# Optimization experiments

Hardware: AMD Instinct MI355X
Metric: run time of the kernel (lower is better)

## Reference

```python
import jax, jax.numpy as jnp
import numpy as np
import math

N_EMBD = 384
N_HEAD = 6
HEAD_DIM = N_EMBD // N_HEAD  # 64
EPS = 1e-5


def apply_rotary_emb(x, cos, sin):
    # x: [B, T, H, D]; cos/sin: [1, T, 1, D//2]
    d = x.shape[3] // 2
    x1, x2 = x[..., :d], x[..., d:]
    y1 = x1 * cos + x2 * sin
    y2 = -x1 * sin + x2 * cos
    return jnp.concatenate([y1, y2], axis=3).astype(x.dtype)


def rms_norm(x):
    # no learned gain, eps inside the sqrt's argument as in the torch code
    return x * jax.lax.rsqrt(jnp.mean(x * x, axis=-1, keepdims=True) + EPS)


def setup_inputs() -> dict:
    key = jax.random.key(0)
    ks = jax.random.split(key, 7)
    B, T = 8, 2048
    x = jax.random.normal(ks[0], (B, T, N_EMBD), dtype=jnp.float32)
    scale = 1.0 / math.sqrt(N_EMBD)
    Wq = jax.random.normal(ks[1], (N_EMBD, N_EMBD), dtype=jnp.float32) * scale
    Wk = jax.random.normal(ks[2], (N_EMBD, N_EMBD), dtype=jnp.float32) * scale
    Wv = jax.random.normal(ks[3], (N_EMBD, N_EMBD), dtype=jnp.float32) * scale
    Wo = jax.random.normal(ks[4], (N_EMBD, N_EMBD), dtype=jnp.float32) * scale
    # RoPE tables: true cos/sin of position*inv_freq
    half = HEAD_DIM // 2
    inv_freq = 1.0 / (10000.0 ** (jnp.arange(half, dtype=jnp.float32) / half))
    t = jnp.arange(T, dtype=jnp.float32)
    freqs = t[:, None] * inv_freq[None, :]  # [T, half]
    cos = jnp.cos(freqs)[None, :, None, :]  # [1, T, 1, half]
    sin = jnp.sin(freqs)[None, :, None, :]
    return {"x": x, "Wq": Wq, "Wk": Wk, "Wv": Wv, "Wo": Wo, "cos": cos, "sin": sin}


def reference(x, Wq, Wk, Wv, Wo, cos, sin):
    B, T, C = x.shape
    H, D = N_HEAD, HEAD_DIM
    # torch Linear: y = x @ W.T (weights stored [out, in])
    q = (x @ Wq.T).reshape(B, T, H, D)
    k = (x @ Wk.T).reshape(B, T, H, D)
    v = (x @ Wv.T).reshape(B, T, H, D)
    q = apply_rotary_emb(q, cos, sin)
    k = apply_rotary_emb(k, cos, sin)
    q = rms_norm(q)
    k = rms_norm(k)
    # attention: [B, H, T, T] scores, full softmax (no causal mask in source)
    att = jnp.einsum("bthd,bshd->bhts", q, k) * (1.0 / math.sqrt(D))
    att = jax.nn.softmax(att, axis=-1)
    y = jnp.einsum("bhts,bshd->bthd", att, v).reshape(B, T, C)
    return y @ Wo.T
```

## Files before the change

### kernel.cpp

```cpp
#include <hip/hip_runtime.h>
#include <hip/hip_bf16.h>
#include <stdint.h>

#define B_ 8
#define T_ 2048
#define C_ 384
#define H_ 6
#define D_ 64
#define M_ (B_*T_)

typedef unsigned short u16;
typedef unsigned int u32;
typedef __attribute__((ext_vector_type(8))) short short8;
typedef __attribute__((ext_vector_type(4))) float floatx4;
typedef __attribute__((ext_vector_type(16))) float floatx16;

#define QSCALE 0.18033688011112042f

__device__ __forceinline__ u16 f2b(float f) {
  union { float f; unsigned u; } x; x.f = f;
  unsigned r = x.u + 0x7fffu + ((x.u >> 16) & 1u);
  return (u16)(r >> 16);
}
__device__ __forceinline__ u32 pack_bf16(float a, float b) {
  union { __hip_bfloat162 h; u32 u; } x;
  x.h = __float22bfloat162_rn(float2{a, b});
  return x.u;
}
__device__ __forceinline__ uint4 pack8(const float4& lo, const float4& hi) {
  uint4 r;
  r.x = pack_bf16(lo.x, lo.y); r.y = pack_bf16(lo.z, lo.w);
  r.z = pack_bf16(hi.x, hi.y); r.w = pack_bf16(hi.z, hi.w);
  return r;
}

__device__ __forceinline__ void plswap(u32& a, u32& b) {
  asm("v_permlane32_swap_b32 %0, %1" : "+v"(a), "+v"(b));
}

__device__ __forceinline__ float fexp2(float x) {
#if __has_builtin(__builtin_amdgcn_exp2f)
  return __builtin_amdgcn_exp2f(x);
#else
  float r; asm("v_exp_f32 %0, %1" : "=v"(r) : "v"(x)); return r;
#endif
}

__device__ __forceinline__ u32 cvtpk(float a, float b) {
  u32 r; asm("v_cvt_pk_bf16_f32 %0, %1, %2" : "=v"(r) : "v"(a), "v"(b)); return r;
}

__device__ __forceinline__ void gl_lds16(const u16* g, u16* l) {
#if __has_builtin(__builtin_amdgcn_global_load_lds)
  __builtin_amdgcn_global_load_lds(
      (const __attribute__((address_space(1))) unsigned int*)g,
      (__attribute__((address_space(3))) unsigned int*)l,
      16, 0, 0);
#else
  *reinterpret_cast<uint4*>(l + (threadIdx.x & 63) * 8) =
      *reinterpret_cast<const uint4*>(g);
#endif
}

__global__ __launch_bounds__(256) void prep_bf16(
    const float* __restrict__ x,
    const float* __restrict__ wq, const float* __restrict__ wk,
    const float* __restrict__ wv, const float* __restrict__ wo,
    u16* __restrict__ xb,
    u16* __restrict__ wqb, u16* __restrict__ wkb,
    u16* __restrict__ wvb, u16* __restrict__ wob)
{
  const int c = blockIdx.x * 256 + threadIdx.x;
  const float* src;
  u16* dst;
  int off;
  if (c < 786432) {
    src = x; dst = xb; off = c;
  } else {
    int t = c - 786432;
    int wsel = t / 18432;
    off = t - wsel * 18432;
    src = (wsel == 0) ? wq : (wsel == 1) ? wk : (wsel == 2) ? wv : wo;
    dst = (wsel == 0) ? wqb : (wsel == 1) ? wkb : (wsel == 2) ? wvb : wob;
  }
  const float4* p = reinterpret_cast<const float4*>(src + (size_t)off * 8);
  float4 lo = p[0], hi = p[1];
  *reinterpret_cast<uint4*>(dst + (size_t)off * 8) = pack8(lo, hi);
}

__global__ __launch_bounds__(256) void qkv_fused(
    const u16* __restrict__ Xb,
    const u16* __restrict__ Wqb, const u16* __restrict__ Wkb, const u16* __restrict__ Wvb,
    const float* __restrict__ cosb, const float* __restrict__ sinb,
    u16* __restrict__ Qo, u16* __restrict__ Ko, u16* __restrict__ Vto)
{
  __shared__ __align__(16) u16 smem[128 * 64 + 3 * 64 * 64];
  u16* As = smem;
  u16* Bs0 = smem + 128 * 64;

  const int id = blockIdx.x;
  const int xcd = id & 7;
  const int s = id >> 3;
  const int mb = xcd * 16 + s / 6;
  const int hh = s % 6;
  const int m0 = mb * 128;
  const int n0 = hh * 64;

  const int tid = threadIdx.x;
  const int w = tid >> 6;
  const int lane = tid & 63;
  const int quad = lane >> 4;
  const int c = lane & 15;

  const u16* Wz[3] = {Wqb, Wkb, Wvb};

  floatx4 acc[3][2][4];
#pragma unroll
  for (int z = 0; z < 3; z++)
#pragma unroll
    for (int i = 0; i < 2; i++)
#pragma unroll
      for (int j = 0; j < 4; j++) acc[z][i][j] = (floatx4){0.f, 0.f, 0.f, 0.f};

  const int lrow = lane >> 3;
  const int lcol = (lane & 7) * 8;

  for (int k0 = 0; k0 < 384; k0 += 64) {
    __syncthreads();
#pragma unroll
    for (int n = 0; n < 4; n++) {
      const int ch = w * 4 + n;
      gl_lds16(Xb + (size_t)(m0 + ch * 8 + lrow) * C_ + k0 + lcol, As + ch * 512);
    }
#pragma unroll
    for (int z = 0; z < 3; z++)
#pragma unroll
      for (int n = 0; n < 2; n++) {
        const int ch = w * 2 + n;
        gl_lds16(Wz[z] + (size_t)(n0 + ch * 8 + lrow) * C_ + k0 + lcol,
                 Bs0 + z * 4096 + ch * 512);
      }
    __syncthreads();

#pragma unroll
    for (int ks = 0; ks < 2; ks++) {
      short8 af2[2];
#pragma unroll
      for (int mi = 0; mi < 2; mi++)
        af2[mi] = *reinterpret_cast<const short8*>(
            As + (w * 32 + mi * 16 + c) * 64 + (ks * 4 + quad) * 8);
#pragma unroll
      for (int z = 0; z < 3; z++) {
#pragma unroll
        for (int ni = 0; ni < 4; ni++) {
          short8 bf = *reinterpret_cast<const short8*>(
              Bs0 + z * 4096 + (ni * 16 + c) * 64 + (ks * 4 + quad) * 8);
#pragma unroll
          for (int mi = 0; mi < 2; mi++)
            acc[z][mi][ni] = __builtin_amdgcn_mfma_f32_16x16x32_bf16(af2[mi], bf, acc[z][mi][ni], 0, 0, 0);
        }
      }
    }
  }

  const int bb2 = m0 >> 11;
  const int tbase = m0 & (T_ - 1);

  {
    const size_t vbase = ((size_t)(bb2 * H_ + hh)) * D_ * T_;
#pragma unroll
    for (int mi = 0; mi < 2; mi++) {
      int t = tbase + w * 32 + mi * 16 + quad * 4;
#pragma unroll
      for (int ni = 0; ni < 4; ni++) {
        int d = ni * 16 + c;
        ushort4 pk;
        pk.x = f2b(acc[2][mi][ni][0]); pk.y = f2b(acc[2][mi][ni][1]);
        pk.z = f2b(acc[2][mi][ni][2]); pk.w = f2b(acc[2][mi][ni][3]);
        *reinterpret_cast<ushort4*>(Vto + vbase + (size_t)d * T_ + t) = pk;
      }
    }
  }

  u16* Ep = smem;
#pragma unroll
  for (int zz = 0; zz < 2; zz++) {
    __syncthreads();
#pragma unroll
    for (int mi = 0; mi < 2; mi++) {
      float ssr[4];
#pragma unroll
      for (int r = 0; r < 4; r++) {
        float s0 = acc[zz][mi][0][r], s1 = acc[zz][mi][1][r];
        float s2 = acc[zz][mi][2][r], s3 = acc[zz][mi][3][r];
        ssr[r] = s0 * s0 + s1 * s1 + s2 * s2 + s3 * s3;
      }
#pragma unroll
      for (int off = 1; off < 16; off <<= 1)
#pragma unroll
        for (int r = 0; r < 4; r++) ssr[r] += __shfl_xor(ssr[r], off, 64);
      int rowb = w * 32 + mi * 16 + quad * 4;
#pragma unroll
      for (int r = 0; r < 4; r++) {
        float scl = rsqrtf(ssr[r] * (1.0f / 64.0f) + 1e-5f);
        if (zz == 0) scl *= QSCALE;
        int t = tbase + rowb + r;
#pragma unroll
        for (int h2 = 0; h2 < 2; h2++) {
          float cs = cosb[t * 32 + h2 * 16 + c];
          float sn = sinb[t * 32 + h2 * 16 + c];
          float x1 = acc[zz][mi][h2][r];
          float x2 = acc[zz][mi][h2 + 2][r];
          Ep[(rowb + r) * 72 + h2 * 16 + c]       = f2b((x1 * cs + x2 * sn) * scl);
          Ep[(rowb + r) * 72 + (h2 + 2) * 16 + c] = f2b((x2 * cs - x1 * sn) * scl);
        }
      }
    }
    __syncthreads();
    {
      int row = tid >> 1, half = tid & 1;
      int t = tbase + row;
      u16* Og = (zz == 0) ? Qo : Ko;
      u16* dst = Og + (((size_t)(bb2 * H_ + hh)) * T_ + t) * D_ + half * 32;
#pragma unroll
      for (int i = 0; i < 4; i++)
        *reinterpret_cast<uint4*>(dst + i * 8) =
            *reinterpret_cast<const uint4*>(Ep + row * 72 + half * 32 + i * 8);
    }
  }
}

__global__ __launch_bounds__(256, 3) void attn_mfma(
    const u16* __restrict__ Qg, const u16* __restrict__ Kg,
    const u16* __restrict__ Vtg, u16* __restrict__ Yg)
{
  __shared__ __align__(16) u16 smem[16384];

  const int tid = threadIdx.x;
  const int w = tid >> 6;
  const int lane = tid & 63;
  const int hi = lane >> 5;
  const int lq = lane & 31;

  const int id = blockIdx.x;
  const int xcd = id & 7;
  const int slot = id >> 3;
  const int bh = xcd * 6 + (slot >> 4);
  const int q0 = (slot & 15) * 128;

  const size_t baseQK = (size_t)bh * T_ * D_;
  const size_t baseV  = (size_t)bh * D_ * T_;

  short8 qf[4];
  {
    const u16* qp = Qg + baseQK + (size_t)(q0 + w * 32 + lq) * D_ + hi * 8;
#pragma unroll
    for (int d = 0; d < 4; d++)
      qf[d] = *reinterpret_cast<const short8*>(qp + d * 16);
  }

  floatx16 z16;
#pragma unroll
  for (int i = 0; i < 16; i++) z16[i] = 0.f;
  short8 vones;
#pragma unroll
  for (int i = 0; i < 8; i++) vones[i] = (short)0x3F80;

  const int sr = tid >> 2;
  const int sch = tid & 3;
  const int r3s = ((sr & 3) << 1) | ((sr >> 2) & 1);
  const int ko0 = sr * 64 + ((sch ^ r3s) * 8);
  const int ko1 = sr * 64 + (((sch + 4) ^ r3s) * 8);
  const int vo0 = 4096 + ko0;
  const int vo1 = 4096 + ko1;
  const u16* kga = Kg + baseQK + (size_t)sr * D_ + sch * 8;
  const u16* vga = Vtg + baseV + (size_t)sr * T_ + sch * 8;

  uint4 ka = *reinterpret_cast<const uint4*>(kga);
  uint4 kb = *reinterpret_cast<const uint4*>(kga + 32);
  uint4 va = *reinterpret_cast<const uint4*>(vga);
  uint4 vb = *reinterpret_cast<const uint4*>(vga + 32);
  *reinterpret_cast<uint4*>(smem + ko0) = ka;
  *reinterpret_cast<uint4*>(smem + ko1) = kb;
  *reinterpret_cast<uint4*>(smem + vo0) = va;
  *reinterpret_cast<uint4*>(smem + vo1) = vb;
  const u16* kload = kga + (size_t)64 * D_;
  const u16* vload = vga + 64;
  ka = *reinterpret_cast<const uint4*>(kload);
  kb = *reinterpret_cast<const uint4*>(kload + 32);
  va = *reinterpret_cast<const uint4*>(vload);
  vb = *reinterpret_cast<const uint4*>(vload + 32);
  kload += (size_t)64 * D_;
  vload += 64;

  floatx16 o0 = z16, o1 = z16;
  floatx16 l_acc = z16;

  const int r3q = ((lq & 3) << 1) | ((lq >> 2) & 1);

  int koff[2][4], voff[2][4];
#pragma unroll
  for (int ds = 0; ds < 4; ds++) {
    const int xr = (ds * 2 + hi) ^ r3q;
    koff[0][ds] = lq * 64 + xr * 8;
    koff[1][ds] = (32 + lq) * 64 + xr * 8;
    voff[0][ds] = 4096 + lq * 64 + xr * 8;
    voff[1][ds] = 4096 + (32 + lq) * 64 + xr * 8;
  }

  for (int kt = 0; kt < 32; kt++) {
    __syncthreads();

    if (kt < 31) {
      u16* wb = smem + (((kt + 1) & 1) << 13);
      *reinterpret_cast<uint4*>(wb + ko0) = ka;
      *reinterpret_cast<uint4*>(wb + ko1) = kb;
      *reinterpret_cast<uint4*>(wb + vo0) = va;
      *reinterpret_cast<uint4*>(wb + vo1) = vb;
      if (kt < 30) {
        ka = *reinterpret_cast<const uint4*>(kload);
        kb = *reinterpret_cast<const uint4*>(kload + 32);
        va = *reinterpret_cast<const uint4*>(vload);
        vb = *reinterpret_cast<const uint4*>(vload + 32);
        kload += (size_t)64 * D_;
        vload += 64;
      }
    }

    const u16* Ksb = smem + ((kt & 1) << 13);

    floatx16 st0, st1;
    __builtin_amdgcn_s_setprio(1);
    {
      short8 kf0 = *reinterpret_cast<const short8*>(Ksb + koff[0][0]);
      short8 kf1 = *reinterpret_cast<const short8*>(Ksb + koff[1][0]);
      st0 = __builtin_amdgcn_mfma_f32_32x32x16_bf16(kf0, qf[0], z16, 0, 0, 0);
      st1 = __builtin_amdgcn_mfma_f32_32x32x16_bf16(kf1, qf[0], z16, 0, 0, 0);
    }
#pragma unroll
    for (int ds = 1; ds < 4; ds++) {
      short8 kf0 = *reinterpret_cast<const short8*>(Ksb + koff[0][ds]);
      short8 kf1 = *reinterpret_cast<const short8*>(Ksb + koff[1][ds]);
      st0 = __builtin_amdgcn_mfma_f32_32x32x16_bf16(kf0, qf[ds], st0, 0, 0, 0);
      st1 = __builtin_amdgcn_mfma_f32_32x32x16_bf16(kf1, qf[ds], st1, 0, 0, 0);
    }
    __builtin_amdgcn_s_setprio(0);

#pragma unroll
    for (int r = 0; r < 16; r++) {
      st0[r] = fexp2(st0[r]);
      st1[r] = fexp2(st1[r]);
    }

    short8 pa[4];
#pragma unroll
    for (int ks = 0; ks < 4; ks++) {
      const floatx16& s = (ks < 2) ? st0 : st1;
      const int rb = (ks & 1) * 8;
      u32 ca = cvtpk(s[rb + 0], s[rb + 1]);
      u32 cb = cvtpk(s[rb + 2], s[rb + 3]);
      u32 cc = cvtpk(s[rb + 4], s[rb + 5]);
      u32 cd = cvtpk(s[rb + 6], s[rb + 7]);
      plswap(ca, cc);
      plswap(cb, cd);
      short8 pf;
      u32* pfu = reinterpret_cast<u32*>(&pf);
      pfu[0] = ca; pfu[1] = cb; pfu[2] = cc; pfu[3] = cd;
      pa[ks] = pf;
    }

    __builtin_amdgcn_s_setprio(1);
#pragma unroll
    for (int ks = 0; ks < 4; ks++) {
      short8 vf0 = *reinterpret_cast<const short8*>(Ksb + voff[0][ks]);
      short8 vf1 = *reinterpret_cast<const short8*>(Ksb + voff[1][ks]);
      o0 = __builtin_amdgcn_mfma_f32_32x32x16_bf16(pa[ks], vf0, o0, 0, 0, 0);
      o1 = __builtin_amdgcn_mfma_f32_32x32x16_bf16(pa[ks], vf1, o1, 0, 0, 0);
    }
#pragma unroll
    for (int ks = 0; ks < 4; ks++)
      l_acc = __builtin_amdgcn_mfma_f32_32x32x16_bf16(pa[ks], vones, l_acc, 0, 0, 0);
    __builtin_amdgcn_s_setprio(0);
  }

  float invr[16];
#pragma unroll
  for (int r = 0; r < 16; r++) invr[r] = __builtin_amdgcn_rcpf(l_acc[r]);

  __syncthreads();
  u16* Ep = smem + w * (32 * 72);
#pragma unroll
  for (int nt = 0; nt < 2; nt++) {
    const floatx16& o = nt ? o1 : o0;
#pragma unroll
    for (int r = 0; r < 16; r++) {
      const int rl = (r & 3) + 8 * (r >> 2) + 4 * hi;
      Ep[rl * 72 + nt * 32 + lq] = f2b(o[r] * invr[r]);
    }
  }
  __syncthreads();
  {
    const int row = tid >> 1, half = tid & 1;
    const u16* src = smem + (row >> 5) * (32 * 72) + (row & 31) * 72 + half * 32;
    const int t = q0 + row;
    const int b = bh / H_, h = bh % H_;
    const size_t yi = ((size_t)b * T_ + t) * C_ + (size_t)h * 64 + half * 32;
#pragma unroll
    for (int i = 0; i < 4; i++)
      *reinterpret_cast<uint4*>(Yg + yi + i * 8) =
          *reinterpret_cast<const uint4*>(src + i * 8);
  }
}

__global__ __launch_bounds__(256) void out_mfma(
    const u16* __restrict__ Xb, const u16* __restrict__ Wfb, float* __restrict__ Og)
{
  __shared__ __align__(16) u16 smem[17408];
  u16* As = smem;
  u16* Bs = smem + 128 * 64;

  const int id = blockIdx.x;
  const int xcd = id & 7;
  const int s = id >> 3;
  const int m0 = (xcd * 16 + s / 6) * 128;
  const int n0 = (s % 6) * 64;

  const int tid = threadIdx.x;
  const int w = tid >> 6;
  const int lane = tid & 63;
  const int quad = lane >> 4;
  const int c = lane & 15;

  floatx4 acc[2][4];
#pragma unroll
  for (int i = 0; i < 2; i++)
#pragma unroll
    for (int j = 0; j < 4; j++) acc[i][j] = (floatx4){0.f, 0.f, 0.f, 0.f};

  const int lrow = lane >> 3;
  const int lcol = (lane & 7) * 8;

  for (int k0 = 0; k0 < 384; k0 += 64) {
    __syncthreads();
#pragma unroll
    for (int n = 0; n < 4; n++) {
      const int ch = w * 4 + n;
      gl_lds16(Xb + (size_t)(m0 + ch * 8 + lrow) * C_ + k0 + lcol, As + ch * 512);
    }
#pragma unroll
    for (int n = 0; n < 2; n++) {
      const int ch = w * 2 + n;
      gl_lds16(Wfb + (size_t)(n0 + ch * 8 + lrow) * C_ + k0 + lcol, Bs + ch * 512);
    }
    __syncthreads();

#pragma unroll
    for (int ks = 0; ks < 2; ks++) {
      short8 af[2], bf[4];
#pragma unroll
      for (int mi = 0; mi < 2; mi++)
        af[mi] = *reinterpret_cast<const short8*>(
            As + (w * 32 + mi * 16 + c) * 64 + (ks * 4 + quad) * 8);
#pragma unroll
      for (int ni = 0; ni < 4; ni++)
        bf[ni] = *reinterpret_cast<const short8*>(
            Bs + (ni * 16 + c) * 64 + (ks * 4 + quad) * 8);
#pragma unroll
      for (int mi = 0; mi < 2; mi++)
#pragma unroll
        for (int ni = 0; ni < 4; ni++)
          acc[mi][ni] = __builtin_amdgcn_mfma_f32_16x16x32_bf16(af[mi], bf[ni], acc[mi][ni], 0, 0, 0);
    }
  }

  __syncthreads();
  float* Ep = reinterpret_cast<float*>(smem) + w * (32 * 68);
#pragma unroll
  for (int mi = 0; mi < 2; mi++)
#pragma unroll
    for (int ni = 0; ni < 4; ni++) {
      int rw = mi * 16 + quad * 4;
      int col = ni * 16 + c;
#pragma unroll
      for (int r = 0; r < 4; r++)
        Ep[(rw + r) * 68 + col] = acc[mi][ni][r];
    }
  __syncthreads();
  {
    int rw2 = lane >> 1, half = lane & 1;
    const float* src = Ep + rw2 * 68 + half * 32;
    float* dst = Og + (size_t)(m0 + w * 32 + rw2) * C_ + n0 + half * 32;
#pragma unroll
    for (int i = 0; i < 8; i++)
      *reinterpret_cast<float4*>(dst + i * 4) =
          *reinterpret_cast<const float4*>(src + i * 4);
  }
}

extern "C" void kernel_launch(void* const* d_in, const int* in_sizes, int n_in,
                              void* d_out, int out_size, void* d_ws, size_t ws_size,
                              hipStream_t stream) {
  (void)in_sizes; (void)n_in; (void)out_size; (void)ws_size;
  const float* x    = (const float*)d_in[0];
  const float* Wq   = (const float*)d_in[1];
  const float* Wk   = (const float*)d_in[2];
  const float* Wv   = (const float*)d_in[3];
  const float* Wo   = (const float*)d_in[4];
  const float* cosb = (const float*)d_in[5];
  const float* sinb = (const float*)d_in[6];

  const size_t MC = (size_t)M_ * C_;
  u16* ws = (u16*)d_ws;
  u16* Q   = ws;
  u16* K   = Q + MC;
  u16* Vt  = K + MC;
  u16* Y   = Vt + MC;
  u16* Xb  = Y;
  u16* Wb  = Y + MC;
  u16* Wqb = Wb;
  u16* Wkb = Wb + 147456;
  u16* Wvb = Wb + 2 * 147456;
  u16* Wob = Wb + 3 * 147456;
  float* out = (float*)d_out;

  prep_bf16<<<3360, 256, 0, stream>>>(x, Wq, Wk, Wv, Wo, Xb, Wqb, Wkb, Wvb, Wob);

  qkv_fused<<<768, 256, 0, stream>>>(Xb, Wqb, Wkb, Wvb, cosb, sinb, Q, K, Vt);

  attn_mfma<<<768, 256, 0, stream>>>(Q, K, Vt, Y);

  out_mfma<<<768, 256, 0, stream>>>(Y, Wob, out);
}
```

Measured before the change: 214.0 us.

## Double-buffer LDS tiles in QKV and output projection GEMMs

Both projection GEMM kernels now hold two shared-memory stage buffers. Each iteration issues the global-to-LDS loads for the next K-slice before running the MFMA work on the current one. This removes one barrier per iteration and is meant to overlap load latency with compute. In exchange, LDS use per block roughly doubles (about 80KB in the QKV kernel), which may cut the number of resident blocks per CU.

```diff
diff --git a/kernel.cpp b/kernel.cpp
--- a/kernel.cpp
+++ b/kernel.cpp
@@ -88,15 +88,15 @@
   *reinterpret_cast<uint4*>(dst + (size_t)off * 8) = pack8(lo, hi);
 }
 
+#define QKV_SBUF 20480
+
 __global__ __launch_bounds__(256) void qkv_fused(
     const u16* __restrict__ Xb,
     const u16* __restrict__ Wqb, const u16* __restrict__ Wkb, const u16* __restrict__ Wvb,
     const float* __restrict__ cosb, const float* __restrict__ sinb,
     u16* __restrict__ Qo, u16* __restrict__ Ko, u16* __restrict__ Vto)
 {
-  __shared__ __align__(16) u16 smem[128 * 64 + 3 * 64 * 64];
-  u16* As = smem;
-  u16* Bs0 = smem + 128 * 64;
+  __shared__ __align__(16) u16 smem[2 * QKV_SBUF];
 
   const int id = blockIdx.x;
   const int xcd = id & 7;
@@ -125,12 +125,12 @@
   const int lrow = lane >> 3;
   const int lcol = (lane & 7) * 8;
 
-  for (int k0 = 0; k0 < 384; k0 += 64) {
-    __syncthreads();
+  auto STAGE = [&](int bb, int k0) {
+    u16* base = smem + bb * QKV_SBUF;
 #pragma unroll
     for (int n = 0; n < 4; n++) {
       const int ch = w * 4 + n;
-      gl_lds16(Xb + (size_t)(m0 + ch * 8 + lrow) * C_ + k0 + lcol, As + ch * 512);
+      gl_lds16(Xb + (size_t)(m0 + ch * 8 + lrow) * C_ + k0 + lcol, base + ch * 512);
     }
 #pragma unroll
     for (int z = 0; z < 3; z++)
@@ -138,10 +138,19 @@
       for (int n = 0; n < 2; n++) {
         const int ch = w * 2 + n;
         gl_lds16(Wz[z] + (size_t)(n0 + ch * 8 + lrow) * C_ + k0 + lcol,
-                 Bs0 + z * 4096 + ch * 512);
+                 base + 8192 + z * 4096 + ch * 512);
       }
-    __syncthreads();
-
+  };
+
+  STAGE(0, 0);
+  __syncthreads();
+
+  for (int i = 0; i < 6; i++) {
+    const int bb = i & 1;
+    if (i < 5) STAGE(bb ^ 1, (i + 1) * 64);
+
+    const u16* As = smem + bb * QKV_SBUF;
+    const u16* Bs0 = As + 8192;
 #pragma unroll
     for (int ks = 0; ks < 2; ks++) {
       short8 af2[2];
@@ -161,6 +170,7 @@
         }
       }
     }
+    if (i < 5) __syncthreads();
   }
 
   const int bb2 = m0 >> 11;
@@ -412,12 +422,12 @@
   }
 }
 
+#define OUT_SBUF 12288
+
 __global__ __launch_bounds__(256) void out_mfma(
     const u16* __restrict__ Xb, const u16* __restrict__ Wfb, float* __restrict__ Og)
 {
-  __shared__ __align__(16) u16 smem[17408];
-  u16* As = smem;
-  u16* Bs = smem + 128 * 64;
+  __shared__ __align__(16) u16 smem[2 * OUT_SBUF];
 
   const int id = blockIdx.x;
   const int xcd = id & 7;
@@ -440,20 +450,30 @@
   const int lrow = lane >> 3;
   const int lcol = (lane & 7) * 8;
 
-  for (int k0 = 0; k0 < 384; k0 += 64) {
-    __syncthreads();
+  auto STAGE = [&](int bb, int k0) {
+    u16* base = smem + bb * OUT_SBUF;
 #pragma unroll
     for (int n = 0; n < 4; n++) {
       const int ch = w * 4 + n;
-      gl_lds16(Xb + (size_t)(m0 + ch * 8 + lrow) * C_ + k0 + lcol, As + ch * 512);
+      gl_lds16(Xb + (size_t)(m0 + ch * 8 + lrow) * C_ + k0 + lcol, base + ch * 512);
     }
 #pragma unroll
     for (int n = 0; n < 2; n++) {
       const int ch = w * 2 + n;
-      gl_lds16(Wfb + (size_t)(n0 + ch * 8 + lrow) * C_ + k0 + lcol, Bs + ch * 512);
-    }
-    __syncthreads();
-
+      gl_lds16(Wfb + (size_t)(n0 + ch * 8 + lrow) * C_ + k0 + lcol,
+               base + 8192 + ch * 512);
+    }
+  };
+
+  STAGE(0, 0);
+  __syncthreads();
+
+  for (int i = 0; i < 6; i++) {
+    const int bb = i & 1;
+    if (i < 5) STAGE(bb ^ 1, (i + 1) * 64);
+
+    const u16* As = smem + bb * OUT_SBUF;
+    const u16* Bs = As + 8192;
 #pragma unroll
     for (int ks = 0; ks < 2; ks++) {
       short8 af[2], bf[4];
@@ -471,6 +491,7 @@
         for (int ni = 0; ni < 4; ni++)
           acc[mi][ni] = __builtin_amdgcn_mfma_f32_16x16x32_bf16(af[mi], bf[ni], acc[mi][ni], 0, 0, 0);
     }
+    if (i < 5) __syncthreads();
   }
 
   __syncthreads();
```

New measurement: 209.7 us (median of 2 runs). -2.0%, faster.
